# Performance work log

Hardware: AMD Instinct MI355X
Metric: run time of the kernel (lower is better)

## Reference

```python
import jax, jax.numpy as jnp
import numpy as np

D = 512
EPS = 1e-5  # torch BatchNorm1d default eps


def swish(x):
    return x * jax.nn.sigmoid(x)


def batchnorm_train(x, gamma, beta):
    # BatchNorm1d in training mode: biased batch stats
    m = jnp.mean(x, axis=0)
    v = jnp.mean((x - m) ** 2, axis=0)
    return gamma * (x - m) / jnp.sqrt(v + EPS) + beta


def setup_inputs() -> dict:
    key = jax.random.key(0)
    k_fea, k_w1, k_w2, k_lerp = jax.random.split(key, 4)
    bs, P = 32768, 8192
    fea = jax.random.normal(k_fea, (bs, D), dtype=jnp.float32)
    # first P rows are the minority (positive) class
    lbl = jnp.concatenate([jnp.ones((P, 1), jnp.int32), jnp.zeros((bs - P, 1), jnp.int32)], axis=0)
    scale = 1.0 / np.sqrt(D)
    W1 = jax.random.normal(k_w1, (D, D), dtype=jnp.float32) * scale
    W2 = jax.random.normal(k_w2, (D, D), dtype=jnp.float32) * scale
    b1 = jnp.zeros((D,), jnp.float32)
    b2 = jnp.zeros((D,), jnp.float32)
    g1 = jnp.ones((D,), jnp.float32)
    g2 = jnp.ones((D,), jnp.float32)
    beta1 = jnp.zeros((D,), jnp.float32)
    beta2 = jnp.zeros((D,), jnp.float32)
    lerp_w = jax.random.uniform(k_lerp, (P, 3), dtype=jnp.float32)
    return dict(fea=fea, lbl=lbl, W1=W1, b1=b1, g1=g1, beta1=beta1,
                W2=W2, b2=b2, g2=g2, beta2=beta2, lerp_w=lerp_w, num_pos=P)


def reference(fea, lbl, W1, b1, g1, beta1, W2, b2, g2, beta2, lerp_w, num_pos):
    # fea_transform: Linear -> BN -> Swish -> Linear -> BN -> Swish
    h = swish(batchnorm_train(fea @ W1 + b1, g1, beta1))
    h = swish(batchnorm_train(h @ W2 + b2, g2, beta2))

    # SMOTE path (training mode): KNN over positive-class features
    pos_idx = jnp.nonzero(lbl[:, 0] > 0, size=num_pos)[0]  # static-size gather
    x = h[pos_idx]                                          # (P, D)
    sq = jnp.sum(x * x, axis=-1)                            # (P,)
    # negative squared pairwise distance; topk largest == nearest
    neg_dist = 2.0 * (x @ x.T) - sq[:, None] - sq[None, :]  # (P, P)
    _, idx = jax.lax.top_k(neg_dist, 3)                     # (P, 3), idx[:,0] == self

    a = x[idx[:, 0]]                                        # (P, D) anchor
    b = x[idx]                                              # (P, 3, D) neighbors
    # torch.lerp(a, b, w) = a + w * (b - a), one random w per (i, j)
    new_fea = a[:, None, :] + lerp_w[..., None] * (b - a[:, None, :])
    new_fea = new_fea.reshape(-1, D)                        # (3P, D), row-major matches i,j loop order

    fea_out = jnp.concatenate([h, new_fea], axis=0)
    lbl_out = jnp.concatenate([lbl, jnp.ones((new_fea.shape[0], 1), lbl.dtype)], axis=0)
    return fea_out, lbl_out
```

## Files before the change

### kernel.cpp

```cpp
#include <hip/hip_runtime.h>
#include <math.h>

#define NEG_INF -3.402823466e38f
#define NSPLIT 8

typedef __attribute__((ext_vector_type(8))) short bf16x8;
typedef __attribute__((ext_vector_type(4))) float f32x4;

__device__ __forceinline__ void gload_lds16(const unsigned short* g, unsigned short* l) {
  __builtin_amdgcn_global_load_lds(
      (const __attribute__((address_space(1))) unsigned int*)g,
      (__attribute__((address_space(3))) unsigned int*)l, 16, 0, 0);
}
__device__ __forceinline__ void gload_lds16f(const float* g, float* l) {
  __builtin_amdgcn_global_load_lds(
      (const __attribute__((address_space(1))) unsigned int*)g,
      (__attribute__((address_space(3))) unsigned int*)l, 16, 0, 0);
}

__device__ __forceinline__ unsigned short f2bf(float f) {
  union { float f; unsigned int u; } a; a.f = f;
  unsigned int u = a.u;
  return (unsigned short)((u + 0x7fffu + ((u >> 16) & 1u)) >> 16);
}

__device__ __forceinline__ void split3_8(f32x4 a, f32x4 b,
                                         bf16x8& hi, bf16x8& md, bf16x8& lo) {
  union { bf16x8 v; unsigned int u[4]; } H, M, L;
  float f[8];
  f[0]=a[0]; f[1]=a[1]; f[2]=a[2]; f[3]=a[3];
  f[4]=b[0]; f[5]=b[1]; f[6]=b[2]; f[7]=b[3];
#pragma unroll
  for (int p = 0; p < 4; ++p) {
    union { float f; unsigned int u; } x0, x1, h0, h1, r0, r1, m0, m1, s0, s1;
    x0.f = f[2*p]; x1.f = f[2*p+1];
    H.u[p] = (x0.u >> 16) | (x1.u & 0xffff0000u);
    h0.u = x0.u & 0xffff0000u; h1.u = x1.u & 0xffff0000u;
    r0.f = x0.f - h0.f;        r1.f = x1.f - h1.f;
    M.u[p] = (r0.u >> 16) | (r1.u & 0xffff0000u);
    m0.u = r0.u & 0xffff0000u; m1.u = r1.u & 0xffff0000u;
    s0.f = r0.f - m0.f;        s1.f = r1.f - m1.f;
    L.u[p] = (s0.u >> 16) | (s1.u & 0xffff0000u);
  }
  hi = H.v; md = M.v; lo = L.v;
}

__global__ __launch_bounds__(256) void split_w_t3(const float* __restrict__ W,
    unsigned short* __restrict__ Th, unsigned short* __restrict__ Tm,
    unsigned short* __restrict__ Tl)
{
  __shared__ float T[64][65];
  int k0 = blockIdx.x * 64, n0 = blockIdx.y * 64;
  int tid = threadIdx.x;
  int r = tid >> 4, c4 = (tid & 15) << 2;
#pragma unroll
  for (int p = 0; p < 4; ++p) {
    int row = r + p * 16;
    float4 v = *(const float4*)&W[(size_t)(k0 + row) * 512 + n0 + c4];
    T[c4 + 0][row] = v.x; T[c4 + 1][row] = v.y;
    T[c4 + 2][row] = v.z; T[c4 + 3][row] = v.w;
  }
  __syncthreads();
  int nr = tid >> 2, kc = (tid & 3) << 4;
#pragma unroll
  for (int u = 0; u < 16; ++u) {
    union { float f; unsigned int u; } x, h, rr, m, ss;
    x.f = T[nr][kc + u];
    unsigned short hb = (unsigned short)(x.u >> 16);
    h.u = x.u & 0xffff0000u;
    rr.f = x.f - h.f;
    unsigned short mb = (unsigned short)(rr.u >> 16);
    m.u = rr.u & 0xffff0000u;
    ss.f = rr.f - m.f;
    unsigned short lb = (unsigned short)(ss.u >> 16);
    size_t o = (size_t)(n0 + nr) * 512 + k0 + kc + u;
    Th[o] = hb; Tm[o] = mb; Tl[o] = lb;
  }
}

__global__ __launch_bounds__(256, 2) void gemm_split3(
    const float* __restrict__ A, const unsigned short* __restrict__ Bth,
    const unsigned short* __restrict__ Btm, const unsigned short* __restrict__ Btl,
    const float* __restrict__ bias, float* __restrict__ C, float* __restrict__ partial)
{
  __shared__ char smem[81920];
  const int tid = threadIdx.x;
  const int w = tid >> 6, lane = tid & 63;
  const int bm = blockIdx.x * 128, bn = blockIdx.y * 128;
  const int fr = lane & 15, fg = lane >> 4;
  const int arow = tid >> 3, acb = (tid & 7) << 4;
  const int brow = tid >> 2, bcb = (tid & 3) << 4;

  f32x4 acc[2][8];
#pragma unroll
  for (int mi = 0; mi < 2; ++mi)
#pragma unroll
    for (int ni = 0; ni < 8; ++ni) acc[mi][ni] = (f32x4){0.f, 0.f, 0.f, 0.f};

  auto STAGE = [&](int buf, int ktf) {
    float* sA = (float*)(smem + buf * 40960);
    unsigned short* sBh = (unsigned short*)(smem + buf * 40960 + 16384);
    unsigned short* sBm = sBh + 4096;
    unsigned short* sBl = sBm + 4096;
#pragma unroll
    for (int p = 0; p < 4; ++p) {
      int row = arow + p * 32;
      int cb = acb ^ ((row & 7) << 4);
      gload_lds16f(&A[(size_t)(bm + row) * 512 + ktf + (cb >> 2)],
                   &sA[row * 32 + (acb >> 2)]);
    }
#pragma unroll
    for (int p = 0; p < 2; ++p) {
      int row = brow + p * 64;
      int cb = bcb ^ (((row >> 1) & 3) << 4);
      int so = row * 32 + (bcb >> 1);
      gload_lds16(&Bth[(size_t)(bn + row) * 512 + ktf + (cb >> 1)], &sBh[so]);
      gload_lds16(&Btm[(size_t)(bn + row) * 512 + ktf + (cb >> 1)], &sBm[so]);
      gload_lds16(&Btl[(size_t)(bn + row) * 512 + ktf + (cb >> 1)], &sBl[so]);
    }
  };

  STAGE(0, 0);
  __syncthreads();
  for (int it = 0; it < 16; ++it) {
    int cur = it & 1;
    if (it + 1 < 16) STAGE(cur ^ 1, (it + 1) * 32);
    float* sA = (float*)(smem + cur * 40960);
    unsigned short* sBh = (unsigned short*)(smem + cur * 40960 + 16384);
    unsigned short* sBm = sBh + 4096;
    unsigned short* sBl = sBm + 4096;
    bf16x8 ah[2], am[2], al[2];
#pragma unroll
    for (int mi = 0; mi < 2; ++mi) {
      int row = w * 32 + mi * 16 + fr;
      int swz = (row & 7) << 4;
      const char* rb = (const char*)(sA + row * 32);
      f32x4 f0 = *(const f32x4*)(rb + ((fg * 32) ^ swz));
      f32x4 f1 = *(const f32x4*)(rb + ((fg * 32 + 16) ^ swz));
      split3_8(f0, f1, ah[mi], am[mi], al[mi]);
    }
#pragma unroll
    for (int ni = 0; ni < 8; ++ni) {
      int row = ni * 16 + fr;
      int off = row * 32 + (((fg * 16) ^ (((row >> 1) & 3) << 4)) >> 1);
      bf16x8 bh  = *(const bf16x8*)&sBh[off];
      bf16x8 bmf = *(const bf16x8*)&sBm[off];
      bf16x8 blf = *(const bf16x8*)&sBl[off];
#pragma unroll
      for (int mi = 0; mi < 2; ++mi) {
        acc[mi][ni] = __builtin_amdgcn_mfma_f32_16x16x32_bf16(al[mi], bh,  acc[mi][ni], 0, 0, 0);
        acc[mi][ni] = __builtin_amdgcn_mfma_f32_16x16x32_bf16(am[mi], bmf, acc[mi][ni], 0, 0, 0);
        acc[mi][ni] = __builtin_amdgcn_mfma_f32_16x16x32_bf16(ah[mi], blf, acc[mi][ni], 0, 0, 0);
        acc[mi][ni] = __builtin_amdgcn_mfma_f32_16x16x32_bf16(am[mi], bh,  acc[mi][ni], 0, 0, 0);
        acc[mi][ni] = __builtin_amdgcn_mfma_f32_16x16x32_bf16(ah[mi], bmf, acc[mi][ni], 0, 0, 0);
        acc[mi][ni] = __builtin_amdgcn_mfma_f32_16x16x32_bf16(ah[mi], bh,  acc[mi][ni], 0, 0, 0);
      }
    }
    __syncthreads();
  }

  float ssv[8], qqv[8];
#pragma unroll
  for (int ni = 0; ni < 8; ++ni) {
    float bno = bias[bn + ni * 16 + fr];
    float s = 0.f, q = 0.f;
#pragma unroll
    for (int mi = 0; mi < 2; ++mi) {
      int row = bm + w * 32 + mi * 16 + fg * 4;
      int col = bn + ni * 16 + fr;
#pragma unroll
      for (int r = 0; r < 4; ++r) {
        float v = acc[mi][ni][r] + bno;
        C[(size_t)(row + r) * 512 + col] = v;
        s += v; q += v * v;
      }
    }
    s += __shfl_xor(s, 16); s += __shfl_xor(s, 32);
    q += __shfl_xor(q, 16); q += __shfl_xor(q, 32);
    ssv[ni] = s; qqv[ni] = q;
  }
  float* ps = (float*)smem;
  if (fg == 0) {
#pragma unroll
    for (int ni = 0; ni < 8; ++ni) {
      ps[((w * 2 + 0) * 8 + ni) * 16 + fr] = ssv[ni];
      ps[((w * 2 + 1) * 8 + ni) * 16 + fr] = qqv[ni];
    }
  }
  __syncthreads();
  if ((w & 1) == 0) {
    int p = w >> 1;
#pragma unroll
    for (int k = 0; k < 4; ++k) {
      int idx = k * 64 + lane;
      int part = idx >> 7;
      int rem = idx & 127;
      int ni = rem >> 4, fr2 = rem & 15;
      float v = ps[(((2 * p) * 2 + part) * 8 + ni) * 16 + fr2]
              + ps[(((2 * p + 1) * 2 + part) * 8 + ni) * 16 + fr2];
      int slot = blockIdx.x * 2 + p;
      partial[(size_t)(slot * 2 + part) * 512 + bn + ni * 16 + fr2] = v;
    }
  }
}

__global__ __launch_bounds__(256) void bn_reduce1(
    const float* __restrict__ partial, float* __restrict__ partial2, int nslot)
{
  int g = blockIdx.x, p = blockIdx.y;
  int per = nslot >> 4;
  int t = threadIdx.x;
#pragma unroll
  for (int cc = 0; cc < 2; ++cc) {
    int c = t + cc * 256;
    float s = 0.f;
    for (int s0 = 0; s0 < per; ++s0) {
      int slot = g * per + s0;
      s += partial[(size_t)(slot * 2 + p) * 512 + c];
    }
    partial2[(size_t)(g * 2 + p) * 512 + c] = s;
  }
}

__global__ void bn_finalize(
    const float* __restrict__ partial2, const float* __restrict__ g,
    const float* __restrict__ beta, float* __restrict__ scale,
    float* __restrict__ shift, int rows)
{
  int c = blockIdx.x * blockDim.x + threadIdx.x;
  if (c >= 512) return;
  float s = 0, s2 = 0;
  for (int b = 0; b < 16; ++b) {
    s  += partial2[(size_t)(b * 2 + 0) * 512 + c];
    s2 += partial2[(size_t)(b * 2 + 1) * 512 + c];
  }
  float m = s / rows;
  float v = s2 / rows - m * m;
  if (v < 0) v = 0;
  float sc = g[c] / sqrtf(v + 1e-5f);
  scale[c] = sc;
  shift[c] = beta[c] - m * sc;
}

__global__ void bn_swish(
    const float* __restrict__ Y, const float* __restrict__ scale,
    const float* __restrict__ shift, float* __restrict__ H, int total4)
{
  int i = blockIdx.x * blockDim.x + threadIdx.x;
  if (i >= total4) return;
  float4 y = ((const float4*)Y)[i];
  int c = (i * 4) & 511;
  float z;
  float4 o;
  z = y.x * scale[c + 0] + shift[c + 0]; o.x = z / (1.f + expf(-z));
  z = y.y * scale[c + 1] + shift[c + 1]; o.y = z / (1.f + expf(-z));
  z = y.z * scale[c + 2] + shift[c + 2]; o.z = z / (1.f + expf(-z));
  z = y.w * scale[c + 3] + shift[c + 3]; o.w = z / (1.f + expf(-z));
  ((float4*)H)[i] = o;
}

__global__ __launch_bounds__(1024) void pos_count(const int* __restrict__ lbl, int n,
                                                  int* __restrict__ cnt,
                                                  int* __restrict__ pos, int P)
{
  int b = blockIdx.x, tid = threadIdx.x;
  int i = b * 1024 + tid;
  if (i < P) pos[i] = 0;
  int pred = (i < n) && (lbl[i] > 0);
  unsigned long long m = __ballot(pred);
  __shared__ int ws[16];
  if ((tid & 63) == 0) ws[tid >> 6] = __popcll(m);
  __syncthreads();
  if (tid == 0) { int s = 0; for (int k = 0; k < 16; ++k) s += ws[k]; cnt[b] = s; }
}

__global__ void pos_prefix(int* __restrict__ cnt, int nb)
{
  if (threadIdx.x == 0) {
    int s = 0;
    for (int b = 0; b < nb; ++b) { int c = cnt[b]; cnt[b] = s; s += c; }
  }
}

__global__ __launch_bounds__(1024) void pos_scatter(const int* __restrict__ lbl, int n,
                                                    const int* __restrict__ cntp,
                                                    int* __restrict__ pos, int P)
{
  int b = blockIdx.x, tid = threadIdx.x;
  int i = b * 1024 + tid;
  int pred = (i < n) && (lbl[i] > 0);
  unsigned long long m = __ballot(pred);
  __shared__ int ws[16];
  int wid = tid >> 6, lane = tid & 63;
  if (lane == 0) ws[wid] = __popcll(m);
  __syncthreads();
  int wbase = 0;
  for (int w2 = 0; w2 < wid; ++w2) wbase += ws[w2];
  int rank = cntp[b] + wbase + __popcll(m & ((1ull << lane) - 1ull));
  if (pred && rank < P) pos[rank] = i;
}

__global__ void gather_sq(const float* __restrict__ H, const int* __restrict__ pos,
                          float* __restrict__ X, unsigned short* __restrict__ Xh,
                          float* __restrict__ sq)
{
  int r = blockIdx.x, t = threadIdx.x;
  int src = pos[r];
  float4 v = *(const float4*)&H[src * 512 + t * 4];
  *(float4*)&X[r * 512 + t * 4] = v;
  ushort4 hv;
  hv.x = f2bf(v.x); hv.y = f2bf(v.y); hv.z = f2bf(v.z); hv.w = f2bf(v.w);
  *(ushort4*)&Xh[r * 512 + t * 4] = hv;
  float s = v.x * v.x + v.y * v.y + v.z * v.z + v.w * v.w;
#pragma unroll
  for (int off = 32; off > 0; off >>= 1) s += __shfl_down(s, off);
  __shared__ float red[2];
  if ((t & 63) == 0) red[t >> 6] = s;
  __syncthreads();
  if (t == 0) sq[r] = red[0] + red[1];
}

__global__ __launch_bounds__(256, 2) void gram8(
    const unsigned short* __restrict__ Xh, const float* __restrict__ sq, int P,
    float* __restrict__ p8v, int* __restrict__ p8j)
{
  __shared__ unsigned short Ah[128 * 64];
  __shared__ unsigned short Bh[128 * 64];
  __shared__ float dl[4][64][17];
  __shared__ float sqj_l[128];

  const int tid = threadIdx.x;
  const int w = tid >> 6, lane = tid & 63;
  const int wr = w >> 1, wc = w & 1;
  const int bi = blockIdx.x * 128;
  const int jchunk = P / NSPLIT;
  const int jlo = blockIdx.y * jchunk;

  const int srow = tid >> 3;
  const int scb  = (tid & 7) << 4;
  const int fr = lane & 15, fg = lane >> 4;

  float t[8]; int ji[8];
#pragma unroll
  for (int q = 0; q < 8; ++q) { t[q] = NEG_INF; ji[q] = 0x7fffffff; }

  for (int jt = 0; jt < jchunk; jt += 128) {
    const int j0 = jlo + jt;
    if (tid < 128) sqj_l[tid] = sq[j0 + tid];
    f32x4 acc[4][4];
#pragma unroll
    for (int mi = 0; mi < 4; ++mi)
#pragma unroll
      for (int ni = 0; ni < 4; ++ni) acc[mi][ni] = (f32x4){0.f, 0.f, 0.f, 0.f};

    for (int kt = 0; kt < 512; kt += 64) {
#pragma unroll
      for (int it = 0; it < 4; ++it) {
        int row = srow + it * 32;
        int cb = scb ^ ((row & 7) << 4);
        gload_lds16(&Xh[(size_t)(bi + row) * 512 + kt + (cb >> 1)],
                    &Ah[row * 64 + (scb >> 1)]);
        gload_lds16(&Xh[(size_t)(j0 + row) * 512 + kt + (cb >> 1)],
                    &Bh[row * 64 + (scb >> 1)]);
      }
      __syncthreads();
#pragma unroll
      for (int ks = 0; ks < 2; ++ks) {
        bf16x8 af[4], bfr[4];
        int kb = ks * 64 + fg * 16;
#pragma unroll
        for (int mi = 0; mi < 4; ++mi) {
          int row = wr * 64 + mi * 16 + fr;
          af[mi] = *(const bf16x8*)&Ah[row * 64 + ((kb ^ ((row & 7) << 4)) >> 1)];
        }
#pragma unroll
        for (int ni = 0; ni < 4; ++ni) {
          int row = wc * 64 + ni * 16 + fr;
          bfr[ni] = *(const bf16x8*)&Bh[row * 64 + ((kb ^ ((row & 7) << 4)) >> 1)];
        }
#pragma unroll
        for (int mi = 0; mi < 4; ++mi)
#pragma unroll
          for (int ni = 0; ni < 4; ++ni)
            acc[mi][ni] = __builtin_amdgcn_mfma_f32_16x16x32_bf16(
                af[mi], bfr[ni], acc[mi][ni], 0, 0, 0);
      }
      __syncthreads();
    }

#pragma unroll
    for (int qn = 0; qn < 4; ++qn) {
      float sqv = sqj_l[wc * 64 + qn * 16 + fr];
#pragma unroll
      for (int mi = 0; mi < 4; ++mi)
#pragma unroll
        for (int r = 0; r < 4; ++r)
          dl[w][mi * 16 + fg * 4 + r][fr] = 2.0f * acc[mi][qn][r] - sqv;
      __syncthreads();
      int jbase = j0 + wc * 64 + qn * 16;
      for (int c = 0; c < 16; ++c) {
        float v = dl[w][lane][c];
        if (v > t[7]) {
          t[7] = v; ji[7] = jbase + c;
#pragma unroll
          for (int q = 7; q > 0; --q) {
            if (t[q] > t[q - 1]) {
              float tv = t[q]; t[q] = t[q - 1]; t[q - 1] = tv;
              int tj = ji[q]; ji[q] = ji[q - 1]; ji[q - 1] = tj;
            }
          }
        }
      }
      __syncthreads();
    }
  }

  int row = bi + wr * 64 + lane;
  int set = blockIdx.y * 2 + wc;
  size_t base = ((size_t)row * (NSPLIT * 2) + set) * 8;
#pragma unroll
  for (int q = 0; q < 8; ++q) { p8v[base + q] = t[q]; p8j[base + q] = ji[q]; }
}

__global__ __launch_bounds__(256) void merge8w(const float* __restrict__ p8v,
                                               const int* __restrict__ p8j,
                                               int* __restrict__ cand, int P)
{
  int row = blockIdx.x * 4 + (threadIdx.x >> 6);
  int lane = threadIdx.x & 63;
  if (row >= P) return;
  const float* v = p8v + (size_t)row * 128;
  const int* j = p8j + (size_t)row * 128;
  float v0 = v[lane * 2], v1 = v[lane * 2 + 1];
  int j0 = j[lane * 2], j1 = j[lane * 2 + 1];
  for (int k = 0; k < 8; ++k) {
    float bv; int bj;
    if (v0 > v1 || (v0 == v1 && j0 < j1)) { bv = v0; bj = j0; }
    else { bv = v1; bj = j1; }
#pragma unroll
    for (int off = 1; off < 64; off <<= 1) {
      float ov = __shfl_xor(bv, off);
      int oj = __shfl_xor(bj, off);
      if (ov > bv || (ov == bv && oj < bj)) { bv = ov; bj = oj; }
    }
    if (lane == 0) cand[row * 8 + k] = bj;
    if (j0 == bj) { v0 = NEG_INF; j0 = 0x7fffffff; }
    if (j1 == bj) { v1 = NEG_INF; j1 = 0x7fffffff; }
  }
}

__global__ __launch_bounds__(64) void rescore(
    const float* __restrict__ X, const float* __restrict__ sq,
    const int* __restrict__ cand, int* __restrict__ idx3)
{
  int i = blockIdx.x;
  int lane = threadIdx.x;
  f32x4 x0 = *(const f32x4*)&X[(size_t)i * 512 + lane * 8];
  f32x4 x1 = *(const f32x4*)&X[(size_t)i * 512 + lane * 8 + 4];
  float d[8]; int cj[8];
#pragma unroll
  for (int c = 0; c < 8; ++c) {
    int j = cand[i * 8 + c];
    cj[c] = j;
    f32x4 y0 = *(const f32x4*)&X[(size_t)j * 512 + lane * 8];
    f32x4 y1 = *(const f32x4*)&X[(size_t)j * 512 + lane * 8 + 4];
    float p = x0.x * y0.x + x0.y * y0.y + x0.z * y0.z + x0.w * y0.w
            + x1.x * y1.x + x1.y * y1.y + x1.z * y1.z + x1.w * y1.w;
#pragma unroll
    for (int off = 32; off > 0; off >>= 1) p += __shfl_xor(p, off);
    d[c] = 2.0f * p - sq[i] - sq[j];
  }
  if (lane == 0) {
    for (int k = 0; k < 3; ++k) {
      int b = 0;
#pragma unroll
      for (int c = 1; c < 8; ++c)
        if (d[c] > d[b] || (d[c] == d[b] && cj[c] < cj[b])) b = c;
      idx3[i * 3 + k] = cj[b];
      d[b] = NEG_INF; cj[b] = 0x7fffffff;
    }
  }
}

__global__ void make_newfea(const float* __restrict__ X, const int* __restrict__ idx3,
                            const float* __restrict__ lw, float* __restrict__ out)
{
  int r = blockIdx.x;
  int i = r / 3, k = r - i * 3;
  int ai = idx3[i * 3 + 0];
  int bi = idx3[i * 3 + k];
  float w = lw[r];
  int t = threadIdx.x;
  float4 av = *(const float4*)&X[ai * 512 + t * 4];
  float4 bv = *(const float4*)&X[bi * 512 + t * 4];
  float4 o;
  o.x = av.x + w * (bv.x - av.x);
  o.y = av.y + w * (bv.y - av.y);
  o.z = av.z + w * (bv.z - av.z);
  o.w = av.w + w * (bv.w - av.w);
  *(float4*)&out[(size_t)r * 512 + t * 4] = o;
}

__global__ void write_lbl(const int* __restrict__ lbl, float* __restrict__ out,
                          int n_in, int n_total)
{
  int i = blockIdx.x * blockDim.x + threadIdx.x;
  if (i < n_total) out[i] = (i < n_in) ? (float)lbl[i] : 1.0f;
}

extern "C" void kernel_launch(void* const* d_in, const int* in_sizes, int n_in,
                              void* d_out, int out_size, void* d_ws, size_t ws_size,
                              hipStream_t stream)
{
  const float* fea   = (const float*)d_in[0];
  const int*   lbl   = (const int*)d_in[1];
  const float* W1    = (const float*)d_in[2];
  const float* b1    = (const float*)d_in[3];
  const float* g1    = (const float*)d_in[4];
  const float* beta1 = (const float*)d_in[5];
  const float* W2    = (const float*)d_in[6];
  const float* b2    = (const float*)d_in[7];
  const float* g2    = (const float*)d_in[8];
  const float* beta2 = (const float*)d_in[9];
  const float* lerp_w = (const float*)d_in[10];

  int bs = in_sizes[0] / 512;
  int P  = in_sizes[10] / 3;
  int n_total = bs + 3 * P;

  float* out_f = (float*)d_out;
  float* Hout = out_f;
  float* newfea = out_f + (size_t)bs * 512;
  float* lbl_out = out_f + (size_t)n_total * 512;

  const size_t MB = 1024 * 1024;
  const size_t KB = 1024;
  char* ws = (char*)d_ws;
  float* Y1 = (float*)ws;
  float* X  = (float*)(ws + 64 * MB);
  unsigned short* W1h = (unsigned short*)(ws + 64 * MB);
  unsigned short* W1m = (unsigned short*)(ws + 64 * MB + 512 * KB);
  unsigned short* W1l = (unsigned short*)(ws + 64 * MB + 1024 * KB);
  unsigned short* W2h = (unsigned short*)(ws + 64 * MB + 1536 * KB);
  unsigned short* W2m = (unsigned short*)(ws + 64 * MB + 2048 * KB);
  unsigned short* W2l = (unsigned short*)(ws + 64 * MB + 2560 * KB);
  float* partial = (float*)(ws + 80 * MB);
  float* scale = (float*)(ws + 82 * MB);
  float* shiftv = scale + 512;
  float* sq = shiftv + 512;
  int* pos = (int*)(sq + 8192);
  int* idx3 = pos + 8192;
  int* cnt = idx3 + 3 * 8192;
  float* partial2 = (float*)(ws + 83 * MB);
  unsigned short* Xh = (unsigned short*)ws;
  float* p8v = (float*)(ws + 8 * MB);
  int*   p8j = (int*)(ws + 12 * MB);
  int*   cand = (int*)(ws + 16 * MB);

  dim3 wgrid(8, 8);
  split_w_t3<<<wgrid, 256, 0, stream>>>(W1, W1h, W1m, W1l);
  split_w_t3<<<wgrid, 256, 0, stream>>>(W2, W2h, W2m, W2l);

  dim3 ggrid(bs / 128, 4);
  int nslot = (bs / 128) * 2;
  dim3 rgrid(16, 2);

  gemm_split3<<<ggrid, 256, 0, stream>>>(fea, W1h, W1m, W1l, b1, Y1, partial);
  bn_reduce1<<<rgrid, 256, 0, stream>>>(partial, partial2, nslot);
  bn_finalize<<<2, 256, 0, stream>>>(partial2, g1, beta1, scale, shiftv, bs);
  bn_swish<<<(bs * 512 / 4 + 255) / 256, 256, 0, stream>>>(Y1, scale, shiftv, Y1, bs * 512 / 4);

  gemm_split3<<<ggrid, 256, 0, stream>>>(Y1, W2h, W2m, W2l, b2, Hout, partial);
  bn_reduce1<<<rgrid, 256, 0, stream>>>(partial, partial2, nslot);
  bn_finalize<<<2, 256, 0, stream>>>(partial2, g2, beta2, scale, shiftv, bs);
  bn_swish<<<(bs * 512 / 4 + 255) / 256, 256, 0, stream>>>(Hout, scale, shiftv, Hout, bs * 512 / 4);

  int nb = (bs + 1023) / 1024;
  pos_count<<<nb, 1024, 0, stream>>>(lbl, bs, cnt, pos, P);
  pos_prefix<<<1, 64, 0, stream>>>(cnt, nb);
  pos_scatter<<<nb, 1024, 0, stream>>>(lbl, bs, cnt, pos, P);
  gather_sq<<<P, 128, 0, stream>>>(Hout, pos, X, Xh, sq);

  dim3 gram_grid(P / 128, NSPLIT);
  gram8<<<gram_grid, 256, 0, stream>>>(Xh, sq, P, p8v, p8j);
  merge8w<<<(P + 3) / 4, 256, 0, stream>>>(p8v, p8j, cand, P);
  rescore<<<P, 64, 0, stream>>>(X, sq, cand, idx3);

  make_newfea<<<3 * P, 128, 0, stream>>>(X, idx3, lerp_w, newfea);
  write_lbl<<<(n_total + 255) / 256, 256, 0, stream>>>(lbl, lbl_out, bs, n_total);
}
```

Before: 465.2 us.

## Exploit Gram matrix symmetry: compute upper-triangle tiles and emit top-8 for both sides

Replaces the row-block by column-split Gram kernel with one that launches only the upper-triangular 128x128 tile pairs. Each tile computes the dot products once and extracts per-row top-8 candidates for the i-block and, via a transposed pass, for the j-block. This roughly halves the MFMA work of the P x P distance matrix. In exchange it adds a per-tile selection pass, a larger candidate buffer (64 sets per row), and a reworked merge kernel that does a 64-way merge of sorted lists, plus a triangular index decode in every block.

```diff
diff --git a/kernel.cpp b/kernel.cpp
--- a/kernel.cpp
+++ b/kernel.cpp
@@ -2,7 +2,6 @@
 #include <math.h>
 
 #define NEG_INF -3.402823466e38f
-#define NSPLIT 8
 
 typedef __attribute__((ext_vector_type(8))) short bf16x8;
 typedef __attribute__((ext_vector_type(4))) float f32x4;
@@ -320,106 +319,184 @@
   if (t == 0) sq[r] = red[0] + red[1];
 }
 
-__global__ __launch_bounds__(256, 2) void gram8(
-    const unsigned short* __restrict__ Xh, const float* __restrict__ sq, int P,
+__global__ __launch_bounds__(256, 3) void gram_sym(
+    const unsigned short* __restrict__ Xh, const float* __restrict__ sq,
     float* __restrict__ p8v, int* __restrict__ p8j)
 {
-  __shared__ unsigned short Ah[128 * 64];
-  __shared__ unsigned short Bh[128 * 64];
-  __shared__ float dl[4][64][17];
-  __shared__ float sqj_l[128];
+  __shared__ char smem[32768];
+  __shared__ float sqi_l[128], sqj_l[128];
+  unsigned short* Ah = (unsigned short*)smem;
+  unsigned short* Bh = (unsigned short*)(smem + 16384);
+  float (*dl)[64][17] = (float (*)[64][17])(void*)smem;
+  float* mv = (float*)smem;
+  int*   mj = (int*)(smem + 8192);
 
   const int tid = threadIdx.x;
   const int w = tid >> 6, lane = tid & 63;
   const int wr = w >> 1, wc = w & 1;
-  const int bi = blockIdx.x * 128;
-  const int jchunk = P / NSPLIT;
-  const int jlo = blockIdx.y * jchunk;
-
+  const int fr = lane & 15, fg = lane >> 4;
   const int srow = tid >> 3;
   const int scb  = (tid & 7) << 4;
-  const int fr = lane & 15, fg = lane >> 4;
-
-  float t[8]; int ji[8];
-#pragma unroll
-  for (int q = 0; q < 8; ++q) { t[q] = NEG_INF; ji[q] = 0x7fffffff; }
-
-  for (int jt = 0; jt < jchunk; jt += 128) {
-    const int j0 = jlo + jt;
-    if (tid < 128) sqj_l[tid] = sq[j0 + tid];
-    f32x4 acc[4][4];
+
+  int t = blockIdx.x;
+  int a = (int)(64.5f - sqrtf(64.5f * 64.5f - 2.0f * (float)t));
+  if (a < 0) a = 0;
+  while (a > 0 && (a * (129 - a)) / 2 > t) --a;
+  while (((a + 1) * (128 - a)) / 2 <= t) ++a;
+  int b = a + (t - (a * (129 - a)) / 2);
+  const int ai0 = a * 128, bj0 = b * 128;
+
+  if (tid < 128) { sqi_l[tid] = sq[ai0 + tid]; sqj_l[tid] = sq[bj0 + tid]; }
+
+  f32x4 acc[4][4];
+#pragma unroll
+  for (int mi = 0; mi < 4; ++mi)
+#pragma unroll
+    for (int ni = 0; ni < 4; ++ni) acc[mi][ni] = (f32x4){0.f, 0.f, 0.f, 0.f};
+
+  for (int kt = 0; kt < 512; kt += 64) {
+#pragma unroll
+    for (int it = 0; it < 4; ++it) {
+      int row = srow + it * 32;
+      int cb = scb ^ ((row & 7) << 4);
+      gload_lds16(&Xh[(size_t)(ai0 + row) * 512 + kt + (cb >> 1)],
+                  &Ah[row * 64 + (scb >> 1)]);
+      gload_lds16(&Xh[(size_t)(bj0 + row) * 512 + kt + (cb >> 1)],
+                  &Bh[row * 64 + (scb >> 1)]);
+    }
+    __syncthreads();
+#pragma unroll
+    for (int ks = 0; ks < 2; ++ks) {
+      bf16x8 af[4], bfr[4];
+      int kb = ks * 64 + fg * 16;
+#pragma unroll
+      for (int mi = 0; mi < 4; ++mi) {
+        int row = wr * 64 + mi * 16 + fr;
+        af[mi] = *(const bf16x8*)&Ah[row * 64 + ((kb ^ ((row & 7) << 4)) >> 1)];
+      }
+#pragma unroll
+      for (int ni = 0; ni < 4; ++ni) {
+        int row = wc * 64 + ni * 16 + fr;
+        bfr[ni] = *(const bf16x8*)&Bh[row * 64 + ((kb ^ ((row & 7) << 4)) >> 1)];
+      }
+#pragma unroll
+      for (int mi = 0; mi < 4; ++mi)
+#pragma unroll
+        for (int ni = 0; ni < 4; ++ni)
+          acc[mi][ni] = __builtin_amdgcn_mfma_f32_16x16x32_bf16(
+              af[mi], bfr[ni], acc[mi][ni], 0, 0, 0);
+    }
+    __syncthreads();
+  }
+
+  float t8[8]; int j8[8];
+#pragma unroll
+  for (int q = 0; q < 8; ++q) { t8[q] = NEG_INF; j8[q] = 0x7fffffff; }
+
+#pragma unroll
+  for (int qn = 0; qn < 4; ++qn) {
+    float sqv = sqj_l[wc * 64 + qn * 16 + fr];
 #pragma unroll
     for (int mi = 0; mi < 4; ++mi)
 #pragma unroll
-      for (int ni = 0; ni < 4; ++ni) acc[mi][ni] = (f32x4){0.f, 0.f, 0.f, 0.f};
-
-    for (int kt = 0; kt < 512; kt += 64) {
-#pragma unroll
-      for (int it = 0; it < 4; ++it) {
-        int row = srow + it * 32;
-        int cb = scb ^ ((row & 7) << 4);
-        gload_lds16(&Xh[(size_t)(bi + row) * 512 + kt + (cb >> 1)],
-                    &Ah[row * 64 + (scb >> 1)]);
-        gload_lds16(&Xh[(size_t)(j0 + row) * 512 + kt + (cb >> 1)],
-                    &Bh[row * 64 + (scb >> 1)]);
+      for (int r = 0; r < 4; ++r)
+        dl[w][mi * 16 + fg * 4 + r][fr] = 2.0f * acc[mi][qn][r] - sqv;
+    __syncthreads();
+    int jbase = bj0 + wc * 64 + qn * 16;
+    for (int c = 0; c < 16; ++c) {
+      float v = dl[w][lane][c];
+      if (v > t8[7]) {
+        t8[7] = v; j8[7] = jbase + c;
+#pragma unroll
+        for (int q = 7; q > 0; --q)
+          if (t8[q] > t8[q - 1]) {
+            float tv = t8[q]; t8[q] = t8[q - 1]; t8[q - 1] = tv;
+            int tj = j8[q]; j8[q] = j8[q - 1]; j8[q - 1] = tj;
+          }
       }
+    }
+    __syncthreads();
+  }
+#pragma unroll
+  for (int q = 0; q < 8; ++q) {
+    mv[(w * 64 + lane) * 8 + q] = t8[q];
+    mj[(w * 64 + lane) * 8 + q] = j8[q];
+  }
+  __syncthreads();
+  if ((w & 1) == 0) {
+    int row = ai0 + (w >> 1) * 64 + lane;
+    const float* v0 = &mv[(w * 64 + lane) * 8];
+    const int*   c0 = &mj[(w * 64 + lane) * 8];
+    const float* v1 = &mv[((w + 1) * 64 + lane) * 8];
+    const int*   c1 = &mj[((w + 1) * 64 + lane) * 8];
+    size_t ob = ((size_t)row * 64 + b) * 8;
+    int h0 = 0, h1 = 0;
+    for (int k = 0; k < 8; ++k) {
+      float a0 = (h0 < 8) ? v0[h0] : NEG_INF;
+      float a1 = (h1 < 8) ? v1[h1] : NEG_INF;
+      int   b0 = (h0 < 8) ? c0[h0] : 0x7fffffff;
+      int   b1 = (h1 < 8) ? c1[h1] : 0x7fffffff;
+      bool take0 = (a0 > a1) || (a0 == a1 && b0 < b1);
+      p8v[ob + k] = take0 ? a0 : a1;
+      p8j[ob + k] = take0 ? b0 : b1;
+      if (take0) ++h0; else ++h1;
+    }
+  }
+
+  if (a != b) {
+    __syncthreads();
+#pragma unroll
+    for (int q = 0; q < 8; ++q) { t8[q] = NEG_INF; j8[q] = 0x7fffffff; }
+#pragma unroll
+    for (int mi = 0; mi < 4; ++mi) {
+      f32x4 sv = *(const f32x4*)&sqi_l[wr * 64 + mi * 16 + fg * 4];
+#pragma unroll
+      for (int ni = 0; ni < 4; ++ni)
+#pragma unroll
+        for (int r = 0; r < 4; ++r)
+          dl[w][ni * 16 + fr][fg * 4 + r] = 2.0f * acc[mi][ni][r] - sv[r];
       __syncthreads();
-#pragma unroll
-      for (int ks = 0; ks < 2; ++ks) {
-        bf16x8 af[4], bfr[4];
-        int kb = ks * 64 + fg * 16;
-#pragma unroll
-        for (int mi = 0; mi < 4; ++mi) {
-          int row = wr * 64 + mi * 16 + fr;
-          af[mi] = *(const bf16x8*)&Ah[row * 64 + ((kb ^ ((row & 7) << 4)) >> 1)];
-        }
-#pragma unroll
-        for (int ni = 0; ni < 4; ++ni) {
-          int row = wc * 64 + ni * 16 + fr;
-          bfr[ni] = *(const bf16x8*)&Bh[row * 64 + ((kb ^ ((row & 7) << 4)) >> 1)];
-        }
-#pragma unroll
-        for (int mi = 0; mi < 4; ++mi)
-#pragma unroll
-          for (int ni = 0; ni < 4; ++ni)
-            acc[mi][ni] = __builtin_amdgcn_mfma_f32_16x16x32_bf16(
-                af[mi], bfr[ni], acc[mi][ni], 0, 0, 0);
-      }
-      __syncthreads();
-    }
-
-#pragma unroll
-    for (int qn = 0; qn < 4; ++qn) {
-      float sqv = sqj_l[wc * 64 + qn * 16 + fr];
-#pragma unroll
-      for (int mi = 0; mi < 4; ++mi)
-#pragma unroll
-        for (int r = 0; r < 4; ++r)
-          dl[w][mi * 16 + fg * 4 + r][fr] = 2.0f * acc[mi][qn][r] - sqv;
-      __syncthreads();
-      int jbase = j0 + wc * 64 + qn * 16;
+      int ibase = ai0 + wr * 64 + mi * 16;
       for (int c = 0; c < 16; ++c) {
         float v = dl[w][lane][c];
-        if (v > t[7]) {
-          t[7] = v; ji[7] = jbase + c;
-#pragma unroll
-          for (int q = 7; q > 0; --q) {
-            if (t[q] > t[q - 1]) {
-              float tv = t[q]; t[q] = t[q - 1]; t[q - 1] = tv;
-              int tj = ji[q]; ji[q] = ji[q - 1]; ji[q - 1] = tj;
+        if (v > t8[7]) {
+          t8[7] = v; j8[7] = ibase + c;
+#pragma unroll
+          for (int q = 7; q > 0; --q)
+            if (t8[q] > t8[q - 1]) {
+              float tv = t8[q]; t8[q] = t8[q - 1]; t8[q - 1] = tv;
+              int tj = j8[q]; j8[q] = j8[q - 1]; j8[q - 1] = tj;
             }
-          }
         }
       }
       __syncthreads();
     }
-  }
-
-  int row = bi + wr * 64 + lane;
-  int set = blockIdx.y * 2 + wc;
-  size_t base = ((size_t)row * (NSPLIT * 2) + set) * 8;
-#pragma unroll
-  for (int q = 0; q < 8; ++q) { p8v[base + q] = t[q]; p8j[base + q] = ji[q]; }
+#pragma unroll
+    for (int q = 0; q < 8; ++q) {
+      mv[(w * 64 + lane) * 8 + q] = t8[q];
+      mj[(w * 64 + lane) * 8 + q] = j8[q];
+    }
+    __syncthreads();
+    if (wr == 0) {
+      int row = bj0 + wc * 64 + lane;
+      const float* v0 = &mv[(w * 64 + lane) * 8];
+      const int*   c0 = &mj[(w * 64 + lane) * 8];
+      const float* v1 = &mv[((w + 2) * 64 + lane) * 8];
+      const int*   c1 = &mj[((w + 2) * 64 + lane) * 8];
+      size_t ob = ((size_t)row * 64 + a) * 8;
+      int h0 = 0, h1 = 0;
+      for (int k = 0; k < 8; ++k) {
+        float a0 = (h0 < 8) ? v0[h0] : NEG_INF;
+        float a1 = (h1 < 8) ? v1[h1] : NEG_INF;
+        int   b0 = (h0 < 8) ? c0[h0] : 0x7fffffff;
+        int   b1 = (h1 < 8) ? c1[h1] : 0x7fffffff;
+        bool take0 = (a0 > a1) || (a0 == a1 && b0 < b1);
+        p8v[ob + k] = take0 ? a0 : a1;
+        p8j[ob + k] = take0 ? b0 : b1;
+        if (take0) ++h0; else ++h1;
+      }
+    }
+  }
 }
 
 __global__ __launch_bounds__(256) void merge8w(const float* __restrict__ p8v,
@@ -429,23 +506,25 @@
   int row = blockIdx.x * 4 + (threadIdx.x >> 6);
   int lane = threadIdx.x & 63;
   if (row >= P) return;
-  const float* v = p8v + (size_t)row * 128;
-  const int* j = p8j + (size_t)row * 128;
-  float v0 = v[lane * 2], v1 = v[lane * 2 + 1];
-  int j0 = j[lane * 2], j1 = j[lane * 2 + 1];
+  const float* v = p8v + (size_t)row * 512 + lane * 8;
+  const int* j = p8j + (size_t)row * 512 + lane * 8;
+  float vv[8]; int jj[8];
+#pragma unroll
+  for (int q = 0; q < 8; ++q) { vv[q] = v[q]; jj[q] = j[q]; }
   for (int k = 0; k < 8; ++k) {
-    float bv; int bj;
-    if (v0 > v1 || (v0 == v1 && j0 < j1)) { bv = v0; bj = j0; }
-    else { bv = v1; bj = j1; }
+    float cv = vv[0]; int cj = jj[0];
 #pragma unroll
     for (int off = 1; off < 64; off <<= 1) {
-      float ov = __shfl_xor(bv, off);
-      int oj = __shfl_xor(bj, off);
-      if (ov > bv || (ov == bv && oj < bj)) { bv = ov; bj = oj; }
-    }
-    if (lane == 0) cand[row * 8 + k] = bj;
-    if (j0 == bj) { v0 = NEG_INF; j0 = 0x7fffffff; }
-    if (j1 == bj) { v1 = NEG_INF; j1 = 0x7fffffff; }
+      float ov = __shfl_xor(cv, off);
+      int oj = __shfl_xor(cj, off);
+      if (ov > cv || (ov == cv && oj < cj)) { cv = ov; cj = oj; }
+    }
+    if (lane == 0) cand[row * 8 + k] = cj;
+    if (jj[0] == cj) {
+#pragma unroll
+      for (int q = 0; q < 7; ++q) { vv[q] = vv[q + 1]; jj[q] = jj[q + 1]; }
+      vv[7] = NEG_INF; jj[7] = 0x7fffffff;
+    }
   }
 }
 
@@ -554,8 +633,8 @@
   float* partial2 = (float*)(ws + 83 * MB);
   unsigned short* Xh = (unsigned short*)ws;
   float* p8v = (float*)(ws + 8 * MB);
-  int*   p8j = (int*)(ws + 12 * MB);
-  int*   cand = (int*)(ws + 16 * MB);
+  int*   p8j = (int*)(ws + 24 * MB);
+  int*   cand = (int*)(ws + 40 * MB);
 
   dim3 wgrid(8, 8);
   split_w_t3<<<wgrid, 256, 0, stream>>>(W1, W1h, W1m, W1l);
@@ -581,8 +660,9 @@
   pos_scatter<<<nb, 1024, 0, stream>>>(lbl, bs, cnt, pos, P);
   gather_sq<<<P, 128, 0, stream>>>(Hout, pos, X, Xh, sq);
 
-  dim3 gram_grid(P / 128, NSPLIT);
-  gram8<<<gram_grid, 256, 0, stream>>>(Xh, sq, P, p8v, p8j);
+  int nbk = P / 128;
+  int ntri = nbk * (nbk + 1) / 2;
+  gram_sym<<<ntri, 256, 0, stream>>>(Xh, sq, p8v, p8j);
   merge8w<<<(P + 3) / 4, 256, 0, stream>>>(p8v, p8j, cand, P);
   rescore<<<P, 64, 0, stream>>>(X, sq, cand, idx3);
 
```

Result: no change. 459.5 us (-1.2%).
